# Kernel optimization log

Hardware: AMD Instinct MI355X
Metric: run time of the kernel (lower is better)

The kernel has to match this reference:

```python
import jax, jax.numpy as jnp
import numpy as np

T, HID, H = 2048, 5120, 16
DN, DR, DV = 128, 64, 128          # qk_nope, qk_rope, v head dims
QL, KVL = 1536, 512                # q_lora_rank, kv_lora_rank
EPS = 1e-6
THETA = 10000.0
SCALE = (DN + DR) ** -0.5          # qk_head_dim^-0.5, no yarn mscale (rope_scaling=None)


def setup_inputs() -> dict:
    key = jax.random.key(0)
    ks = jax.random.split(key, 6)
    s = 0.02  # weight init scale for numerical stability
    return {
        "positions": jnp.arange(T, dtype=jnp.int64) if jax.config.jax_enable_x64 else jnp.arange(T, dtype=jnp.int32),
        "hidden_states": jax.random.normal(ks[0], (T, HID), dtype=jnp.float32),
        "w_fused": jax.random.normal(ks[1], (HID, QL + KVL + DR), dtype=jnp.float32) * s,
        "w_qb": jax.random.normal(ks[2], (QL, H * (DN + DR)), dtype=jnp.float32) * s,
        "w_kvb": jax.random.normal(ks[3], (KVL, H * (DN + DV)), dtype=jnp.float32) * s,
        "w_o": jax.random.normal(ks[4], (H * DV, HID), dtype=jnp.float32) * s,
        "qa_ln_w": jnp.ones((QL,), dtype=jnp.float32),
        "kva_ln_w": jnp.ones((KVL,), dtype=jnp.float32),
    }


def rmsnorm(x, w):
    return x * jax.lax.rsqrt(jnp.mean(x * x, axis=-1, keepdims=True) + EPS) * w


def rope_interleaved(x, cos, sin):
    # non-neox (is_neox_style=False): rotate interleaved pairs
    # x [..., d], cos/sin broadcastable to [..., d/2]
    shp = x.shape
    x = x.reshape(shp[:-1] + (shp[-1] // 2, 2))
    x1, x2 = x[..., 0], x[..., 1]
    o = jnp.stack([x1 * cos - x2 * sin, x2 * cos + x1 * sin], axis=-1)
    return o.reshape(shp)


def reference(positions, hidden_states, w_fused, w_qb, w_kvb, w_o, qa_ln_w, kva_ln_w):
    # fused QKV-A projection: [T, QL + KVL + DR]
    qkv = hidden_states @ w_fused
    q_a = qkv[:, :QL]
    kv_a = qkv[:, QL:QL + KVL]
    k_pe = qkv[:, QL + KVL:]                      # [T, DR]

    # LoRA-Q up-projection
    q = (rmsnorm(q_a, qa_ln_w) @ w_qb).reshape(T, H, DN + DR)
    q_nope, q_pe = q[..., :DN], q[..., DN:]       # [T,H,DN], [T,H,DR]

    # compressed KV latent
    kv_lat = rmsnorm(kv_a, kva_ln_w)              # [T, KVL]

    # RoPE (deepseek non-neox)
    inv_freq = 1.0 / (THETA ** (jnp.arange(0, DR, 2, dtype=jnp.float32) / DR))
    freqs = positions.astype(jnp.float32)[:, None] * inv_freq   # [T, DR/2]
    cos, sin = jnp.cos(freqs), jnp.sin(freqs)
    q_pe = rope_interleaved(q_pe, cos[:, None, :], sin[:, None, :])
    k_pe = rope_interleaved(k_pe, cos, sin)

    # weight absorption: kv_b weight [KVL, H, DN+DV] -> w_kc, w_vc
    w_kvb_r = w_kvb.reshape(KVL, H, DN + DV)
    w_kc = w_kvb_r[..., :DN]                      # [KVL, H, DN]
    w_vc = w_kvb_r[..., DN:]                      # [KVL, H, DV]
    q_nope_abs = jnp.einsum('thd,lhd->thl', q_nope, w_kc)   # [T,H,KVL]

    # MQA over compressed cache: head_dim = KVL + DR, 1 kv head
    q_full = jnp.concatenate([q_nope_abs, q_pe], axis=-1)    # [T,H,KVL+DR]
    k_full = jnp.concatenate([kv_lat, k_pe], axis=-1)        # [T,KVL+DR]
    scores = jnp.einsum('thd,sd->hts', q_full, k_full) * SCALE
    idx = jnp.arange(T)
    causal = idx[:, None] >= idx[None, :]
    scores = jnp.where(causal[None], scores, jnp.finfo(scores.dtype).min)
    p = jax.nn.softmax(scores, axis=-1)                      # [H,T,T]

    o_lat = jnp.einsum('hts,sl->thl', p, kv_lat)             # [T,H,KVL]
    o = jnp.einsum('thl,lhv->thv', o_lat, w_vc)              # [T,H,DV]
    return o.reshape(T, H * DV) @ w_o                        # [T, HID]
```

## Files before the change

### kernel.cpp

```cpp
#include <hip/hip_runtime.h>
#include <math.h>

typedef unsigned short u16;
typedef __bf16 v8bf __attribute__((ext_vector_type(8)));
typedef float   v4f  __attribute__((ext_vector_type(4)));

#define T_SEQ 2048
#define HID   5120
#define NH    16
#define DN    128
#define DR    64
#define DV    128
#define QL    1536
#define KVL   512
#define QKV_N (QL + KVL + DR)
#define QB_N  (NH * (DN + DR))
#define KVB_N (NH * (DN + DV))
#define KFULL (KVL + DR)
#define OD    (NH * DV)
#define SCALE_C 0.07216878364870322f
#define ROPE_K  0.28782313662425576f

#define KIMG_U16 18688
#define VIMG_U16 17408

__device__ __forceinline__ u16 f2b(float f) {
    unsigned int u = __float_as_uint(f);
    return (u16)((u + 0x7fffu + ((u >> 16) & 1u)) >> 16);
}

__device__ __forceinline__ size_t qft_idx(int h, int t, int d) {
    return ((((size_t)h * 128 + (t >> 4)) * 72 + (d >> 3)) * 16 + (t & 15)) * 8 + (d & 7);
}

#define ROR_F(x, CTRL) __uint_as_float(__builtin_amdgcn_update_dpp( \
    0, (int)__float_as_uint(x), CTRL, 0xf, 0xf, true))

#if __has_builtin(__builtin_amdgcn_global_load_lds)
#define ASYNC_CP16(gp, lp) __builtin_amdgcn_global_load_lds( \
    (__attribute__((address_space(1))) void*)(gp),           \
    (__attribute__((address_space(3))) void*)(lp), 16, 0, 0)
#else
#define ASYNC_CP16(gp, lp) do { *(uint4*)(lp) = *(const uint4*)(gp); } while (0)
#endif

__global__ __launch_bounds__(256) void cvt_bf16(
    const float* __restrict__ in, u16* __restrict__ out, int n4)
{
    int i = blockIdx.x * 256 + threadIdx.x;
    if (i < n4) {
        float4 v = ((const float4*)in)[i];
        ushort4 o;
        o.x = f2b(v.x); o.y = f2b(v.y); o.z = f2b(v.z); o.w = f2b(v.w);
        ((ushort4*)out)[i] = o;
    }
}

__global__ __launch_bounds__(256) void transcvt(
    const float* __restrict__ in, u16* __restrict__ out,
    int ldin, int col0, int zcol, long out_z, int Kd)
{
    __shared__ u16 tile[32][33];
    const int bk = blockIdx.x * 32, bn = blockIdx.y * 32, z = blockIdx.z;
    const int r = threadIdx.x >> 3, cg = (threadIdx.x & 7) * 4;
    const float4 v = *(const float4*)(in + (size_t)(bk + r) * ldin + col0 + (size_t)z * zcol + bn + cg);
    tile[r][cg + 0] = f2b(v.x); tile[r][cg + 1] = f2b(v.y);
    tile[r][cg + 2] = f2b(v.z); tile[r][cg + 3] = f2b(v.w);
    __syncthreads();
    ushort4 o;
    o.x = tile[cg + 0][r]; o.y = tile[cg + 1][r];
    o.z = tile[cg + 2][r]; o.w = tile[cg + 3][r];
    *(ushort4*)(out + (size_t)z * out_z + (size_t)(bn + r) * Kd + bk + cg) = o;
}

__global__ __launch_bounds__(256, 2) void gemm_bt(
    const u16* __restrict__ A, const u16* __restrict__ Bt,
    float* __restrict__ C, int M, int N, int K)
{
    __shared__ u16 As[128 * 32], Bs[128 * 32];
    const int tid = threadIdx.x, lane = tid & 63, wave = tid >> 6;
    const int g = lane >> 4, l15 = lane & 15;
    const int bm = blockIdx.y * 128, bn = blockIdx.x * 128;
    const int wm = (wave & 1) * 64, wn = (wave >> 1) * 64;
    const int srow = tid >> 2, skq = (tid & 3) * 8;
    v4f acc[4][4];
#pragma unroll
    for (int i = 0; i < 4; ++i)
#pragma unroll
        for (int j = 0; j < 4; ++j) acc[i][j] = (v4f){0.f, 0.f, 0.f, 0.f};

    for (int k0 = 0; k0 < K; k0 += 32) {
        ASYNC_CP16(A  + (size_t)(bm + srow) * K + k0 + skq,      &As[tid * 8]);
        ASYNC_CP16(A  + (size_t)(bm + 64 + srow) * K + k0 + skq, &As[2048 + tid * 8]);
        ASYNC_CP16(Bt + (size_t)(bn + srow) * K + k0 + skq,      &Bs[tid * 8]);
        ASYNC_CP16(Bt + (size_t)(bn + 64 + srow) * K + k0 + skq, &Bs[2048 + tid * 8]);
        __syncthreads();
        v8bf af[4], bq[4];
#pragma unroll
        for (int mi = 0; mi < 4; ++mi) af[mi] = *(const v8bf*)&As[(wm + mi * 16 + l15) * 32 + g * 8];
#pragma unroll
        for (int ni = 0; ni < 4; ++ni) bq[ni] = *(const v8bf*)&Bs[(wn + ni * 16 + l15) * 32 + g * 8];
#pragma unroll
        for (int mi = 0; mi < 4; ++mi)
#pragma unroll
            for (int ni = 0; ni < 4; ++ni)
                acc[mi][ni] = __builtin_amdgcn_mfma_f32_16x16x32_bf16(af[mi], bq[ni], acc[mi][ni], 0, 0, 0);
        __syncthreads();
    }
#pragma unroll
    for (int mi = 0; mi < 4; ++mi)
#pragma unroll
        for (int ni = 0; ni < 4; ++ni) {
            const int col = bn + wn + ni * 16 + l15;
            if (col < N) {
#pragma unroll
                for (int r = 0; r < 4; ++r)
                    C[(size_t)(bm + wm + mi * 16 + g * 4 + r) * N + col] = acc[mi][ni][r];
            }
        }
}

__global__ __launch_bounds__(256, 2) void gemm_vc(
    const u16* __restrict__ o_lat, const u16* __restrict__ wvcT,
    u16* __restrict__ o_mid)
{
    __shared__ u16 As[128 * 32], Bs[128 * 32];
    const int tid = threadIdx.x, lane = tid & 63, wave = tid >> 6;
    const int g = lane >> 4, l15 = lane & 15;
    const int h = blockIdx.y;
    const int bm = blockIdx.x * 128;
    const u16* A  = o_lat + (size_t)h * T_SEQ * 512;
    const u16* Bt = wvcT + (size_t)h * 128 * 512;
    const int wm = (wave & 1) * 64, wn = (wave >> 1) * 64;
    const int srow = tid >> 2, skq = (tid & 3) * 8;
    v4f acc[4][4];
#pragma unroll
    for (int i = 0; i < 4; ++i)
#pragma unroll
        for (int j = 0; j < 4; ++j) acc[i][j] = (v4f){0.f, 0.f, 0.f, 0.f};

    for (int k0 = 0; k0 < 512; k0 += 32) {
        ASYNC_CP16(A  + (size_t)(bm + srow) * 512 + k0 + skq,      &As[tid * 8]);
        ASYNC_CP16(A  + (size_t)(bm + 64 + srow) * 512 + k0 + skq, &As[2048 + tid * 8]);
        ASYNC_CP16(Bt + (size_t)(srow) * 512 + k0 + skq,           &Bs[tid * 8]);
        ASYNC_CP16(Bt + (size_t)(64 + srow) * 512 + k0 + skq,      &Bs[2048 + tid * 8]);
        __syncthreads();
        v8bf af[4], bq[4];
#pragma unroll
        for (int mi = 0; mi < 4; ++mi) af[mi] = *(const v8bf*)&As[(wm + mi * 16 + l15) * 32 + g * 8];
#pragma unroll
        for (int ni = 0; ni < 4; ++ni) bq[ni] = *(const v8bf*)&Bs[(wn + ni * 16 + l15) * 32 + g * 8];
#pragma unroll
        for (int mi = 0; mi < 4; ++mi)
#pragma unroll
            for (int ni = 0; ni < 4; ++ni)
                acc[mi][ni] = __builtin_amdgcn_mfma_f32_16x16x32_bf16(af[mi], bq[ni], acc[mi][ni], 0, 0, 0);
        __syncthreads();
    }
#pragma unroll
    for (int mi = 0; mi < 4; ++mi)
#pragma unroll
        for (int ni = 0; ni < 4; ++ni)
#pragma unroll
            for (int r = 0; r < 4; ++r)
                o_mid[(size_t)(bm + wm + mi * 16 + g * 4 + r) * OD + h * 128 + wn + ni * 16 + l15] =
                    f2b(acc[mi][ni][r]);
}

__global__ __launch_bounds__(256) void norm_rope_kernel(
    const float* __restrict__ qkv, const float* __restrict__ qa_w,
    const float* __restrict__ kva_w, const int* __restrict__ positions,
    u16* __restrict__ qanorm, u16* __restrict__ k_img, u16* __restrict__ v_img)
{
    const int t = blockIdx.x, tid = threadIdx.x;
    const float* row = qkv + (size_t)t * QKV_N;
    float sq = 0.f, skv = 0.f;
    for (int i = tid; i < QL; i += 256)  { const float v = row[i];      sq  = fmaf(v, v, sq); }
    for (int i = tid; i < KVL; i += 256) { const float v = row[QL + i]; skv = fmaf(v, v, skv); }
#pragma unroll
    for (int off = 32; off >= 1; off >>= 1) {
        sq  += __shfl_down(sq, off, 64);
        skv += __shfl_down(skv, off, 64);
    }
    __shared__ float red[2][4];
    __shared__ float rs[2];
    const int wv = tid >> 6;
    if ((tid & 63) == 0) { red[0][wv] = sq; red[1][wv] = skv; }
    __syncthreads();
    if (tid == 0) {
        const float a = red[0][0] + red[0][1] + red[0][2] + red[0][3];
        const float b = red[1][0] + red[1][1] + red[1][2] + red[1][3];
        rs[0] = rsqrtf(a / (float)QL + 1e-6f);
        rs[1] = rsqrtf(b / (float)KVL + 1e-6f);
    }
    __syncthreads();
    const float rq = rs[0], rkv = rs[1];
    for (int i = tid; i < QL; i += 256)
        qanorm[(size_t)t * QL + i] = f2b(row[i] * rq * qa_w[i]);
    const int kt = t >> 5, r = t & 31;
    u16* krow = k_img + (size_t)kt * KIMG_U16 + (size_t)r * 584;
    u16* vcol = v_img + (size_t)kt * VIMG_U16 + r;
    for (int i = tid; i < KVL; i += 256) {
        const u16 b = f2b(row[QL + i] * rkv * kva_w[i]);
        krow[i] = b;
        vcol[(size_t)i * 34] = b;
    }
    if (tid < 32) {
        const float pos = (float)positions[t];
        const float inv = __expf(-(float)tid * ROPE_K);
        float s, c;
        __sincosf(pos * inv, &s, &c);
        const float x1 = row[QL + KVL + 2 * tid];
        const float x2 = row[QL + KVL + 2 * tid + 1];
        krow[KVL + 2 * tid]     = f2b(x1 * c - x2 * s);
        krow[KVL + 2 * tid + 1] = f2b(x2 * c + x1 * s);
    }
}

__global__ __launch_bounds__(256) void cast_qnope(
    const float* __restrict__ qmat, u16* __restrict__ qn_bf)
{
    const int t = blockIdx.x, tid = threadIdx.x;
#pragma unroll
    for (int i = 0; i < 2; ++i) {
        const int p4 = (tid + i * 256) * 4;
        const int h = p4 >> 7, d = p4 & 127;
        const float4 v = *(const float4*)(qmat + (size_t)t * QB_N + h * (DN + DR) + d);
        ushort4 o;
        o.x = f2b(v.x); o.y = f2b(v.y); o.z = f2b(v.z); o.w = f2b(v.w);
        *(ushort4*)(qn_bf + ((size_t)h * T_SEQ + t) * DN + d) = o;
    }
}

__global__ __launch_bounds__(256) void cast_wkc(
    const float* __restrict__ w_kvb, u16* __restrict__ wkc_bf)
{
    const int gid = blockIdx.x * 256 + threadIdx.x;
    const int p4 = gid * 4;
    const int h = p4 >> 16, rem = p4 & 65535, l = rem >> 7, d = rem & 127;
    const float4 v = *(const float4*)(w_kvb + (size_t)l * KVB_N + h * (DN + DV) + d);
    ushort4 o;
    o.x = f2b(v.x); o.y = f2b(v.y); o.z = f2b(v.z); o.w = f2b(v.w);
    *(ushort4*)(wkc_bf + (size_t)p4) = o;
}

__global__ __launch_bounds__(256, 2) void gemm_qabs(
    const u16* __restrict__ qn_bf, const u16* __restrict__ wkc_bf,
    u16* __restrict__ qfT)
{
    __shared__ u16 As[128 * 32], Bs[128 * 32];
    const int tid = threadIdx.x, lane = tid & 63, wave = tid >> 6;
    const int g = lane >> 4, l15 = lane & 15;
    const int h = blockIdx.z;
    const int bm = blockIdx.y * 128, bn = blockIdx.x * 128;
    const u16* A  = qn_bf + (size_t)h * T_SEQ * DN;
    const u16* Bt = wkc_bf + (size_t)h * KVL * DN;
    const int wm = (wave & 1) * 64, wn = (wave >> 1) * 64;
    const int srow = tid >> 2, skq = (tid & 3) * 8;
    v4f acc[4][4];
#pragma unroll
    for (int i = 0; i < 4; ++i)
#pragma unroll
        for (int j = 0; j < 4; ++j) acc[i][j] = (v4f){0.f, 0.f, 0.f, 0.f};

    for (int k0 = 0; k0 < DN; k0 += 32) {
        ASYNC_CP16(A  + (size_t)(bm + srow) * DN + k0 + skq,      &As[tid * 8]);
        ASYNC_CP16(A  + (size_t)(bm + 64 + srow) * DN + k0 + skq, &As[2048 + tid * 8]);
        ASYNC_CP16(Bt + (size_t)(bn + srow) * DN + k0 + skq,      &Bs[tid * 8]);
        ASYNC_CP16(Bt + (size_t)(bn + 64 + srow) * DN + k0 + skq, &Bs[2048 + tid * 8]);
        __syncthreads();
        v8bf af[4], bq[4];
#pragma unroll
        for (int mi = 0; mi < 4; ++mi) af[mi] = *(const v8bf*)&As[(wm + mi * 16 + l15) * 32 + g * 8];
#pragma unroll
        for (int ni = 0; ni < 4; ++ni) bq[ni] = *(const v8bf*)&Bs[(wn + ni * 16 + l15) * 32 + g * 8];
#pragma unroll
        for (int mi = 0; mi < 4; ++mi)
#pragma unroll
            for (int ni = 0; ni < 4; ++ni)
                acc[mi][ni] = __builtin_amdgcn_mfma_f32_16x16x32_bf16(af[mi], bq[ni], acc[mi][ni], 0, 0, 0);
        __syncthreads();
    }
#pragma unroll
    for (int mi = 0; mi < 4; ++mi)
#pragma unroll
        for (int ni = 0; ni < 4; ++ni)
#pragma unroll
            for (int r = 0; r < 4; ++r) {
                const int t = bm + wm + mi * 16 + g * 4 + r;
                const int d = bn + wn + ni * 16 + l15;
                qfT[qft_idx(h, t, d)] = f2b(acc[mi][ni][r] * SCALE_C);
            }
}

__global__ __launch_bounds__(256) void rope_qpe_kernel(
    const float* __restrict__ q, const int* __restrict__ positions,
    u16* __restrict__ qfT)
{
    const int t = blockIdx.x, tid = threadIdx.x;
    const float pos = (float)positions[t];
    for (int p = tid; p < NH * 32; p += 256) {
        const int h = p >> 5, i = p & 31;
        const float inv = __expf(-(float)i * ROPE_K);
        float s, c;
        __sincosf(pos * inv, &s, &c);
        const float* src = q + (size_t)t * QB_N + h * (DN + DR) + DN;
        const float x1 = src[2 * i], x2 = src[2 * i + 1];
        qfT[qft_idx(h, t, KVL + 2 * i)]     = f2b(SCALE_C * (x1 * c - x2 * s));
        qfT[qft_idx(h, t, KVL + 2 * i + 1)] = f2b(SCALE_C * (x2 * c + x1 * s));
    }
}

__global__ __launch_bounds__(256, 2) void attn_mfma(
    const u16* __restrict__ qfT, const u16* __restrict__ k_img,
    const u16* __restrict__ v_img, u16* __restrict__ o_lat)
{
    __shared__ u16 ks_s[32 * 584];
    __shared__ u16 vt_s[512 * 34];
    __shared__ u16 pt_s[64 * 34];
    __shared__ __align__(16) float alpha_s[64];
    __shared__ __align__(16) float lr_s[64];
    __shared__ __align__(16) unsigned flags_s[4];
    const int h = blockIdx.y;
    const int s = (((blockIdx.x >> 1) + 5 * h) & 15);
    const int tile = (blockIdx.x & 1) ? (31 - s) : s;
    const int qt0 = tile * 64;
    const int nk = 2 * tile + 2;
    const int tid = threadIdx.x, lane = tid & 63, wave = tid >> 6;
    const int g = lane >> 4, l15 = lane & 15;

    const u16* qp = qfT + (size_t)(h * 128 + (qt0 >> 4) + wave) * 9216 + g * 128 + l15 * 8;

    auto STAGE_K = [&](int kt) {
        const char* src = (const char*)(k_img + (size_t)kt * KIMG_U16);
        char* dst = (char*)ks_s;
#pragma unroll
        for (int i = 0; i < 9; ++i)
            ASYNC_CP16(src + (tid + i * 256) * 16, dst + (tid + i * 256) * 16);
        if (tid < 32)
            ASYNC_CP16(src + (2304 + tid) * 16, dst + (2304 + tid) * 16);
    };
    auto STAGE_V = [&](int kt) {
        const char* src = (const char*)(v_img + (size_t)kt * VIMG_U16);
        char* dst = (char*)vt_s;
#pragma unroll
        for (int i = 0; i < 8; ++i)
            ASYNC_CP16(src + (tid + i * 256) * 16, dst + (tid + i * 256) * 16);
        if (tid < 128)
            ASYNC_CP16(src + (2048 + tid) * 16, dst + (2048 + tid) * 16);
    };

    v4f acc[4][8];
#pragma unroll
    for (int m = 0; m < 4; ++m)
#pragma unroll
        for (int n = 0; n < 8; ++n) acc[m][n] = (v4f){0.f, 0.f, 0.f, 0.f};
    float mr[4] = {-1e30f, -1e30f, -1e30f, -1e30f};
    float lrr[4] = {0.f, 0.f, 0.f, 0.f};

    STAGE_K(0);
    STAGE_V(0);
    asm volatile("s_waitcnt vmcnt(0)" ::: "memory");
    __syncthreads();

    for (int kt = 0; kt < nk; ++kt) {
        const int kt0 = kt * 32;
        v4f s0 = (v4f){0.f, 0.f, 0.f, 0.f}, s1 = (v4f){0.f, 0.f, 0.f, 0.f};
#pragma unroll
        for (int half = 0; half < 2; ++half) {
            v8bf aq[9];
#pragma unroll
            for (int c = 0; c < 9; ++c)
                aq[c] = *(const v8bf*)(qp + (half * 9 + c) * 512);
#pragma unroll
            for (int c = 0; c < 9; ++c) {
                const int o = (half * 9 + c) * 32 + g * 8;
                const v8bf b0 = *(const v8bf*)(ks_s + l15 * 584 + o);
                const v8bf b1 = *(const v8bf*)(ks_s + (16 + l15) * 584 + o);
                s0 = __builtin_amdgcn_mfma_f32_16x16x32_bf16(aq[c], b0, s0, 0, 0, 0);
                s1 = __builtin_amdgcn_mfma_f32_16x16x32_bf16(aq[c], b1, s1, 0, 0, 0);
            }
        }
        {
            const int qr = qt0 + wave * 16 + g * 4;
            const int kc0 = kt0 + l15, kc1 = kt0 + 16 + l15;
            float al[4];
            unsigned resc = 0;
#pragma unroll
            for (int r = 0; r < 4; ++r) {
                const float sv0 = (kc0 <= qr + r) ? s0[r] : -1e30f;
                const float sv1 = (kc1 <= qr + r) ? s1[r] : -1e30f;
                float v = fmaxf(sv0, sv1);
                v = fmaxf(v, ROR_F(v, 0x128));
                v = fmaxf(v, ROR_F(v, 0x124));
                v = fmaxf(v, ROR_F(v, 0x122));
                v = fmaxf(v, ROR_F(v, 0x121));
                const float mx = fmaxf(mr[r], v);
                al[r] = __expf(mr[r] - mx);
                resc |= (mx != mr[r]) ? 1u : 0u;
                const float p0 = __expf(sv0 - mx);
                const float p1 = __expf(sv1 - mx);
                pt_s[(wave * 16 + g * 4 + r) * 34 + l15]      = f2b(p0);
                pt_s[(wave * 16 + g * 4 + r) * 34 + 16 + l15] = f2b(p1);
                float ss = p0 + p1;
                ss += ROR_F(ss, 0x128);
                ss += ROR_F(ss, 0x124);
                ss += ROR_F(ss, 0x122);
                ss += ROR_F(ss, 0x121);
                mr[r] = mx;
                lrr[r] = lrr[r] * al[r] + ss;
            }
            const unsigned any = (__ballot(resc) != 0ull) ? 1u : 0u;
            if (l15 == 0) {
                float4 a4;
                a4.x = al[0]; a4.y = al[1]; a4.z = al[2]; a4.w = al[3];
                *(float4*)(alpha_s + wave * 16 + g * 4) = a4;
            }
            if (lane == 0) flags_s[wave] = any;
        }
        __syncthreads();
        if (kt + 1 < nk) STAGE_K(kt + 1);
        {
            v8bf vb[8];
#pragma unroll
            for (int n = 0; n < 8; ++n)
                vb[n] = *(const v8bf*)(vt_s + (wave * 128 + n * 16 + l15) * 34 + g * 8);
            const uint4 flg = *(const uint4*)flags_s;
            const unsigned fl[4] = {flg.x, flg.y, flg.z, flg.w};
#pragma unroll
            for (int m = 0; m < 4; ++m) {
                const float4 am = *(const float4*)(alpha_s + m * 16 + g * 4);
                const v8bf pa = *(const v8bf*)(pt_s + (m * 16 + l15) * 34 + g * 8);
                if (fl[m]) {
#pragma unroll
                    for (int n = 0; n < 8; ++n) {
                        acc[m][n][0] *= am.x; acc[m][n][1] *= am.y;
                        acc[m][n][2] *= am.z; acc[m][n][3] *= am.w;
                    }
                }
#pragma unroll
                for (int n = 0; n < 8; ++n)
                    acc[m][n] = __builtin_amdgcn_mfma_f32_16x16x32_bf16(pa, vb[n], acc[m][n], 0, 0, 0);
            }
        }
        if (kt + 1 < nk) {
            __syncthreads();
            STAGE_V(kt + 1);
            asm volatile("s_waitcnt vmcnt(0)" ::: "memory");
            __syncthreads();
        }
    }
    if (l15 == 0) {
        float4 l4;
        l4.x = lrr[0]; l4.y = lrr[1]; l4.z = lrr[2]; l4.w = lrr[3];
        *(float4*)(lr_s + wave * 16 + g * 4) = l4;
    }
    __syncthreads();
#pragma unroll
    for (int m = 0; m < 4; ++m) {
        const float4 lm = *(const float4*)(lr_s + m * 16 + g * 4);
        const float li0 = 1.f / lm.x, li1 = 1.f / lm.y, li2 = 1.f / lm.z, li3 = 1.f / lm.w;
        u16* op = o_lat + ((size_t)h * T_SEQ + qt0 + m * 16 + g * 4) * 512 + wave * 128 + l15;
#pragma unroll
        for (int n = 0; n < 8; ++n) {
            op[0 * 512 + n * 16] = f2b(acc[m][n][0] * li0);
            op[1 * 512 + n * 16] = f2b(acc[m][n][1] * li1);
            op[2 * 512 + n * 16] = f2b(acc[m][n][2] * li2);
            op[3 * 512 + n * 16] = f2b(acc[m][n][3] * li3);
        }
    }
}

extern "C" void kernel_launch(void* const* d_in, const int* in_sizes, int n_in,
                              void* d_out, int out_size, void* d_ws, size_t ws_size,
                              hipStream_t stream)
{
    const int*   positions = (const int*)d_in[0];
    const float* hs        = (const float*)d_in[1];
    const float* w_fused   = (const float*)d_in[2];
    const float* w_qb      = (const float*)d_in[3];
    const float* w_kvb     = (const float*)d_in[4];
    const float* w_o       = (const float*)d_in[5];
    const float* qa_w      = (const float*)d_in[6];
    const float* kva_w     = (const float*)d_in[7];
    float* out = (float*)d_out;
    char*  ws  = (char*)d_ws;

    char* R0 = ws;
    char* R1 = R0 + 38010880;
    char* R2 = R1 + 17301504;
    char* R3 = R2 + 25165824;
    char* R4 = R3 + 2097152;
    char* R5 = R4 + 2392064;
    char* R6 = R5 + 2228224;

    u16*   wfT    = (u16*)R0;
    u16*   wqbT   = (u16*)(R0 + 22282240);
    u16*   qanorm = (u16*)(R0 + 31719424);
    u16*   o_lat  = (u16*)R0;
    float* qkv    = (float*)R1;
    u16*   qn_bf  = (u16*)R1;
    u16*   wkc_bf = (u16*)(R1 + 8388608);
    u16*   o_mid  = (u16*)R1;
    u16*   hs_bf  = (u16*)R2;
    float* qmat   = (float*)R2;
    u16*   woT    = (u16*)R2;
    u16*   wvcT   = (u16*)R3;
    u16*   k_img  = (u16*)R4;
    u16*   v_img  = (u16*)R5;
    u16*   qfT    = (u16*)R6;

    cvt_bf16<<<(T_SEQ * HID / 4 + 255) / 256, 256, 0, stream>>>(hs, hs_bf, T_SEQ * HID / 4);
    transcvt<<<dim3(HID / 32, QKV_N / 32, 1), 256, 0, stream>>>(w_fused, wfT, QKV_N, 0, 0, 0, HID);
    gemm_bt<<<dim3((QKV_N + 127) / 128, T_SEQ / 128), 256, 0, stream>>>(
        hs_bf, wfT, qkv, T_SEQ, QKV_N, HID);
    transcvt<<<dim3(QL / 32, QB_N / 32, 1), 256, 0, stream>>>(w_qb, wqbT, QB_N, 0, 0, 0, QL);
    norm_rope_kernel<<<T_SEQ, 256, 0, stream>>>(qkv, qa_w, kva_w, positions, qanorm, k_img, v_img);
    gemm_bt<<<dim3(QB_N / 128, T_SEQ / 128), 256, 0, stream>>>(
        qanorm, wqbT, qmat, T_SEQ, QB_N, QL);
    cast_qnope<<<T_SEQ, 256, 0, stream>>>(qmat, qn_bf);
    cast_wkc<<<1024, 256, 0, stream>>>(w_kvb, wkc_bf);
    gemm_qabs<<<dim3(KVL / 128, T_SEQ / 128, NH), 256, 0, stream>>>(qn_bf, wkc_bf, qfT);
    rope_qpe_kernel<<<T_SEQ, 256, 0, stream>>>(qmat, positions, qfT);
    transcvt<<<dim3(KVL / 32, DV / 32, NH), 256, 0, stream>>>(
        w_kvb, wvcT, KVB_N, DN, DN + DV, (long)DV * KVL, KVL);
    attn_mfma<<<dim3(32, NH), 256, 0, stream>>>(qfT, k_img, v_img, o_lat);
    gemm_vc<<<dim3(T_SEQ / 128, NH), 256, 0, stream>>>(o_lat, wvcT, o_mid);
    transcvt<<<dim3(OD / 32, HID / 32, 1), 256, 0, stream>>>(w_o, woT, HID, 0, 0, 0, OD);
    gemm_bt<<<dim3(HID / 128, T_SEQ / 128), 256, 0, stream>>>(
        o_mid, woT, out, T_SEQ, HID, OD);
}
```

Measured before the change: 781.9 us.

## Store V in MFMA fragment layout, load directly to registers, fuse q_pe RoPE

```diff
diff --git a/kernel.cpp b/kernel.cpp
--- a/kernel.cpp
+++ b/kernel.cpp
@@ -22,7 +22,7 @@
 #define ROPE_K  0.28782313662425576f
 
 #define KIMG_U16 18688
-#define VIMG_U16 17408
+#define VFRAG_U16 16384
 
 __device__ __forceinline__ u16 f2b(float f) {
     unsigned int u = __float_as_uint(f);
@@ -170,7 +170,7 @@
 __global__ __launch_bounds__(256) void norm_rope_kernel(
     const float* __restrict__ qkv, const float* __restrict__ qa_w,
     const float* __restrict__ kva_w, const int* __restrict__ positions,
-    u16* __restrict__ qanorm, u16* __restrict__ k_img, u16* __restrict__ v_img)
+    u16* __restrict__ qanorm, u16* __restrict__ k_img, u16* __restrict__ v_frag)
 {
     const int t = blockIdx.x, tid = threadIdx.x;
     const float* row = qkv + (size_t)t * QKV_N;
@@ -197,28 +197,29 @@
     const float rq = rs[0], rkv = rs[1];
     for (int i = tid; i < QL; i += 256)
         qanorm[(size_t)t * QL + i] = f2b(row[i] * rq * qa_w[i]);
-    const int kt = t >> 5, r = t & 31;
-    u16* krow = k_img + (size_t)kt * KIMG_U16 + (size_t)r * 584;
-    u16* vcol = v_img + (size_t)kt * VIMG_U16 + r;
+    const int kt = t >> 5, c = t & 31;
+    u16* krow = k_img + (size_t)kt * KIMG_U16 + (size_t)c * 584;
+    u16* vbase = v_frag + (size_t)kt * VFRAG_U16 + (c >> 3) * 128 + (c & 7);
     for (int i = tid; i < KVL; i += 256) {
         const u16 b = f2b(row[QL + i] * rkv * kva_w[i]);
         krow[i] = b;
-        vcol[(size_t)i * 34] = b;
+        vbase[(size_t)(i >> 4) * 512 + (size_t)(i & 15) * 8] = b;
     }
     if (tid < 32) {
         const float pos = (float)positions[t];
         const float inv = __expf(-(float)tid * ROPE_K);
-        float s, c;
-        __sincosf(pos * inv, &s, &c);
+        float s, cc;
+        __sincosf(pos * inv, &s, &cc);
         const float x1 = row[QL + KVL + 2 * tid];
         const float x2 = row[QL + KVL + 2 * tid + 1];
-        krow[KVL + 2 * tid]     = f2b(x1 * c - x2 * s);
-        krow[KVL + 2 * tid + 1] = f2b(x2 * c + x1 * s);
-    }
-}
-
-__global__ __launch_bounds__(256) void cast_qnope(
-    const float* __restrict__ qmat, u16* __restrict__ qn_bf)
+        krow[KVL + 2 * tid]     = f2b(x1 * cc - x2 * s);
+        krow[KVL + 2 * tid + 1] = f2b(x2 * cc + x1 * s);
+    }
+}
+
+__global__ __launch_bounds__(256) void cast_rope(
+    const float* __restrict__ qmat, const int* __restrict__ positions,
+    u16* __restrict__ qn_bf, u16* __restrict__ qfT)
 {
     const int t = blockIdx.x, tid = threadIdx.x;
 #pragma unroll
@@ -229,6 +230,17 @@
         ushort4 o;
         o.x = f2b(v.x); o.y = f2b(v.y); o.z = f2b(v.z); o.w = f2b(v.w);
         *(ushort4*)(qn_bf + ((size_t)h * T_SEQ + t) * DN + d) = o;
+    }
+    const float pos = (float)positions[t];
+    for (int p = tid; p < NH * 32; p += 256) {
+        const int h = p >> 5, i = p & 31;
+        const float inv = __expf(-(float)i * ROPE_K);
+        float s, c;
+        __sincosf(pos * inv, &s, &c);
+        const float* src = qmat + (size_t)t * QB_N + h * (DN + DR) + DN;
+        const float x1 = src[2 * i], x2 = src[2 * i + 1];
+        qfT[qft_idx(h, t, KVL + 2 * i)]     = f2b(SCALE_C * (x1 * c - x2 * s));
+        qfT[qft_idx(h, t, KVL + 2 * i + 1)] = f2b(SCALE_C * (x2 * c + x1 * s));
     }
 }
 
@@ -293,30 +305,11 @@
             }
 }
 
-__global__ __launch_bounds__(256) void rope_qpe_kernel(
-    const float* __restrict__ q, const int* __restrict__ positions,
-    u16* __restrict__ qfT)
-{
-    const int t = blockIdx.x, tid = threadIdx.x;
-    const float pos = (float)positions[t];
-    for (int p = tid; p < NH * 32; p += 256) {
-        const int h = p >> 5, i = p & 31;
-        const float inv = __expf(-(float)i * ROPE_K);
-        float s, c;
-        __sincosf(pos * inv, &s, &c);
-        const float* src = q + (size_t)t * QB_N + h * (DN + DR) + DN;
-        const float x1 = src[2 * i], x2 = src[2 * i + 1];
-        qfT[qft_idx(h, t, KVL + 2 * i)]     = f2b(SCALE_C * (x1 * c - x2 * s));
-        qfT[qft_idx(h, t, KVL + 2 * i + 1)] = f2b(SCALE_C * (x2 * c + x1 * s));
-    }
-}
-
 __global__ __launch_bounds__(256, 2) void attn_mfma(
     const u16* __restrict__ qfT, const u16* __restrict__ k_img,
-    const u16* __restrict__ v_img, u16* __restrict__ o_lat)
+    const u16* __restrict__ v_frag, u16* __restrict__ o_lat)
 {
     __shared__ u16 ks_s[32 * 584];
-    __shared__ u16 vt_s[512 * 34];
     __shared__ u16 pt_s[64 * 34];
     __shared__ __align__(16) float alpha_s[64];
     __shared__ __align__(16) float lr_s[64];
@@ -340,15 +333,6 @@
         if (tid < 32)
             ASYNC_CP16(src + (2304 + tid) * 16, dst + (2304 + tid) * 16);
     };
-    auto STAGE_V = [&](int kt) {
-        const char* src = (const char*)(v_img + (size_t)kt * VIMG_U16);
-        char* dst = (char*)vt_s;
-#pragma unroll
-        for (int i = 0; i < 8; ++i)
-            ASYNC_CP16(src + (tid + i * 256) * 16, dst + (tid + i * 256) * 16);
-        if (tid < 128)
-            ASYNC_CP16(src + (2048 + tid) * 16, dst + (2048 + tid) * 16);
-    };
 
     v4f acc[4][8];
 #pragma unroll
@@ -359,13 +343,13 @@
     float lrr[4] = {0.f, 0.f, 0.f, 0.f};
 
     STAGE_K(0);
-    STAGE_V(0);
     asm volatile("s_waitcnt vmcnt(0)" ::: "memory");
     __syncthreads();
 
     for (int kt = 0; kt < nk; ++kt) {
         const int kt0 = kt * 32;
-        v4f s0 = (v4f){0.f, 0.f, 0.f, 0.f}, s1 = (v4f){0.f, 0.f, 0.f, 0.f};
+        v4f s0a = (v4f){0.f, 0.f, 0.f, 0.f}, s0b = s0a, s1a = s0a, s1b = s0a;
+        __builtin_amdgcn_s_setprio(1);
 #pragma unroll
         for (int half = 0; half < 2; ++half) {
             v8bf aq[9];
@@ -377,9 +361,21 @@
                 const int o = (half * 9 + c) * 32 + g * 8;
                 const v8bf b0 = *(const v8bf*)(ks_s + l15 * 584 + o);
                 const v8bf b1 = *(const v8bf*)(ks_s + (16 + l15) * 584 + o);
-                s0 = __builtin_amdgcn_mfma_f32_16x16x32_bf16(aq[c], b0, s0, 0, 0, 0);
-                s1 = __builtin_amdgcn_mfma_f32_16x16x32_bf16(aq[c], b1, s1, 0, 0, 0);
+                if (half == 0) {
+                    s0a = __builtin_amdgcn_mfma_f32_16x16x32_bf16(aq[c], b0, s0a, 0, 0, 0);
+                    s1a = __builtin_amdgcn_mfma_f32_16x16x32_bf16(aq[c], b1, s1a, 0, 0, 0);
+                } else {
+                    s0b = __builtin_amdgcn_mfma_f32_16x16x32_bf16(aq[c], b0, s0b, 0, 0, 0);
+                    s1b = __builtin_amdgcn_mfma_f32_16x16x32_bf16(aq[c], b1, s1b, 0, 0, 0);
+                }
             }
+        }
+        __builtin_amdgcn_s_setprio(0);
+        v8bf vb[8];
+        {
+            const u16* vf = v_frag + (size_t)(kt * 32 + wave * 8) * 512 + lane * 8;
+#pragma unroll
+            for (int n = 0; n < 8; ++n) vb[n] = *(const v8bf*)(vf + n * 512);
         }
         {
             const int qr = qt0 + wave * 16 + g * 4;
@@ -388,8 +384,8 @@
             unsigned resc = 0;
 #pragma unroll
             for (int r = 0; r < 4; ++r) {
-                const float sv0 = (kc0 <= qr + r) ? s0[r] : -1e30f;
-                const float sv1 = (kc1 <= qr + r) ? s1[r] : -1e30f;
+                const float sv0 = (kc0 <= qr + r) ? (s0a[r] + s0b[r]) : -1e30f;
+                const float sv1 = (kc1 <= qr + r) ? (s1a[r] + s1b[r]) : -1e30f;
                 float v = fmaxf(sv0, sv1);
                 v = fmaxf(v, ROR_F(v, 0x128));
                 v = fmaxf(v, ROR_F(v, 0x124));
@@ -421,12 +417,9 @@
         __syncthreads();
         if (kt + 1 < nk) STAGE_K(kt + 1);
         {
-            v8bf vb[8];
-#pragma unroll
-            for (int n = 0; n < 8; ++n)
-                vb[n] = *(const v8bf*)(vt_s + (wave * 128 + n * 16 + l15) * 34 + g * 8);
             const uint4 flg = *(const uint4*)flags_s;
             const unsigned fl[4] = {flg.x, flg.y, flg.z, flg.w};
+            __builtin_amdgcn_s_setprio(1);
 #pragma unroll
             for (int m = 0; m < 4; ++m) {
                 const float4 am = *(const float4*)(alpha_s + m * 16 + g * 4);
@@ -442,10 +435,9 @@
                 for (int n = 0; n < 8; ++n)
                     acc[m][n] = __builtin_amdgcn_mfma_f32_16x16x32_bf16(pa, vb[n], acc[m][n], 0, 0, 0);
             }
+            __builtin_amdgcn_s_setprio(0);
         }
         if (kt + 1 < nk) {
-            __syncthreads();
-            STAGE_V(kt + 1);
             asm volatile("s_waitcnt vmcnt(0)" ::: "memory");
             __syncthreads();
         }
@@ -492,7 +484,7 @@
     char* R3 = R2 + 25165824;
     char* R4 = R3 + 2097152;
     char* R5 = R4 + 2392064;
-    char* R6 = R5 + 2228224;
+    char* R6 = R5 + 2097152;
 
     u16*   wfT    = (u16*)R0;
     u16*   wqbT   = (u16*)(R0 + 22282240);
@@ -507,7 +499,7 @@
     u16*   woT    = (u16*)R2;
     u16*   wvcT   = (u16*)R3;
     u16*   k_img  = (u16*)R4;
-    u16*   v_img  = (u16*)R5;
+    u16*   v_frag = (u16*)R5;
     u16*   qfT    = (u16*)R6;
 
     cvt_bf16<<<(T_SEQ * HID / 4 + 255) / 256, 256, 0, stream>>>(hs, hs_bf, T_SEQ * HID / 4);
@@ -515,16 +507,15 @@
     gemm_bt<<<dim3((QKV_N + 127) / 128, T_SEQ / 128), 256, 0, stream>>>(
         hs_bf, wfT, qkv, T_SEQ, QKV_N, HID);
     transcvt<<<dim3(QL / 32, QB_N / 32, 1), 256, 0, stream>>>(w_qb, wqbT, QB_N, 0, 0, 0, QL);
-    norm_rope_kernel<<<T_SEQ, 256, 0, stream>>>(qkv, qa_w, kva_w, positions, qanorm, k_img, v_img);
+    norm_rope_kernel<<<T_SEQ, 256, 0, stream>>>(qkv, qa_w, kva_w, positions, qanorm, k_img, v_frag);
     gemm_bt<<<dim3(QB_N / 128, T_SEQ / 128), 256, 0, stream>>>(
         qanorm, wqbT, qmat, T_SEQ, QB_N, QL);
-    cast_qnope<<<T_SEQ, 256, 0, stream>>>(qmat, qn_bf);
+    cast_rope<<<T_SEQ, 256, 0, stream>>>(qmat, positions, qn_bf, qfT);
     cast_wkc<<<1024, 256, 0, stream>>>(w_kvb, wkc_bf);
     gemm_qabs<<<dim3(KVL / 128, T_SEQ / 128, NH), 256, 0, stream>>>(qn_bf, wkc_bf, qfT);
-    rope_qpe_kernel<<<T_SEQ, 256, 0, stream>>>(qmat, positions, qfT);
     transcvt<<<dim3(KVL / 32, DV / 32, NH), 256, 0, stream>>>(
         w_kvb, wvcT, KVB_N, DN, DN + DV, (long)DV * KVL, KVL);
-    attn_mfma<<<dim3(32, NH), 256, 0, stream>>>(qfT, k_img, v_img, o_lat);
+    attn_mfma<<<dim3(32, NH), 256, 0, stream>>>(qfT, k_img, v_frag, o_lat);
     gemm_vc<<<dim3(T_SEQ / 128, NH), 256, 0, stream>>>(o_lat, wvcT, o_mid);
     transcvt<<<dim3(OD / 32, HID / 32, 1), 256, 0, stream>>>(w_o, woT, HID, 0, 0, 0, OD);
     gemm_bt<<<dim3(HID / 128, T_SEQ / 128), 256, 0, stream>>>(
```

After: 718.3 us. 8.1% less time.
